# Performance work log

Measured on AMD Instinct MI355X. Metric: run time of the kernel, lower is better.

Reference implementation:

```python
import jax, jax.numpy as jnp
from jax import lax
import numpy as np

# ---- constants (from Coords2Elec init kwargs) ----
BOX = 128          # box_size
RES = 1.0          # resolution (Angstrom / voxel)
EPS_IN = 6.5
EPS_OUT = 79.0
ION = 1.0          # ion_size
WAT = 1.4          # wat_size (water probe radius)
ASIGMA = 2.0
KAPPA02 = 0.8486   # debye_length kwarg, passed to solver as kappa0^2
QCONV = 7046.52    # charge_conv
D = 2              # gaussian sharpness divisor
W = 9              # scatter support window per axis (covers ~2.7 sigma)
N_ITER = 20        # Jacobi sweeps for the Poisson-Boltzmann solve

# staggered-grid offsets for the 4 eps channels: face-centered x/y/z + ion grid
OFFSETS = ((0.5, 0.0, 0.0), (0.0, 0.5, 0.0), (0.0, 0.0, 0.5), (0.5, 0.5, 0.5))


def _scatter_gauss(coords, sigma, mask, offset):
    """Scatter per-atom Gaussian density onto a staggered [B,BOX,BOX,BOX] grid.
    coords [B,N,3], sigma [B,N], mask [B,N], offset: 3 floats in voxel units."""
    B, N, _ = coords.shape
    off = jnp.asarray(offset, coords.dtype)
    offs = jnp.arange(W)
    # window base index so that grid node positions (idx+off)*RES bracket the atom
    base = jnp.floor(coords / RES - off).astype(jnp.int32) - W // 2     # [B,N,3]
    idx = base[..., None] + offs                                         # [B,N,3,W]
    gpos = (idx.astype(coords.dtype) + off[None, None, :, None]) * RES   # [B,N,3,W]
    d2 = (gpos - coords[..., None]) ** 2
    wax = jnp.exp(-d2 / (2.0 * sigma[:, :, None, None] ** 2))            # [B,N,3,W]
    w = (wax[:, :, 0, :, None, None] * wax[:, :, 1, None, :, None]
         * wax[:, :, 2, None, None, :]) * mask[:, :, None, None, None]   # [B,N,W,W,W]
    b_idx = jnp.broadcast_to(jnp.arange(B)[:, None, None, None, None], w.shape)
    ix = jnp.broadcast_to(idx[:, :, 0, :, None, None], w.shape)
    iy = jnp.broadcast_to(idx[:, :, 1, None, :, None], w.shape)
    iz = jnp.broadcast_to(idx[:, :, 2, None, None, :], w.shape)
    grid = jnp.zeros((B, BOX, BOX, BOX), coords.dtype)
    return grid.at[b_idx, ix, iy, iz].add(w, mode='drop')


def _scatter_q(coords, charge, mask):
    """Trilinear scatter of per-atom charges onto node grid [B,BOX,BOX,BOX]."""
    B, N, _ = coords.shape
    u = coords / RES
    i0 = jnp.floor(u).astype(jnp.int32)                 # [B,N,3]
    f = u - i0
    wpair = jnp.stack([1.0 - f, f], -1)                 # [B,N,3,2]
    ipair = jnp.stack([i0, i0 + 1], -1)                 # [B,N,3,2]
    w = (wpair[:, :, 0, :, None, None] * wpair[:, :, 1, None, :, None]
         * wpair[:, :, 2, None, None, :]) * (charge * mask)[:, :, None, None, None]
    b_idx = jnp.broadcast_to(jnp.arange(B)[:, None, None, None, None], w.shape)
    ix = jnp.broadcast_to(ipair[:, :, 0, :, None, None], w.shape)
    iy = jnp.broadcast_to(ipair[:, :, 1, None, :, None], w.shape)
    iz = jnp.broadcast_to(ipair[:, :, 2, None, None, :], w.shape)
    grid = jnp.zeros((B, BOX, BOX, BOX), coords.dtype)
    return grid.at[b_idx, ix, iy, iz].add(w, mode='drop')


def _face_nb(a, axis):
    """Face eps of the (i-1) cell along axis; boundary padded with EPS_OUT."""
    lead = jnp.full_like(lax.slice_in_dim(a, 0, 1, axis=axis), EPS_OUT)
    return jnp.concatenate([lead, lax.slice_in_dim(a, 0, a.shape[axis] - 1, axis=axis)], axis=axis)


def _phi_nb(phi, axis, d):
    """Neighbor potential phi[i+d] along spatial axis, zero (Dirichlet) outside."""
    z = jnp.zeros_like(lax.slice_in_dim(phi, 0, 1, axis=axis))
    if d > 0:
        return jnp.concatenate([lax.slice_in_dim(phi, 1, phi.shape[axis], axis=axis), z], axis=axis)
    return jnp.concatenate([z, lax.slice_in_dim(phi, 0, phi.shape[axis] - 1, axis=axis)], axis=axis)


def _qeps2phi(Q, Eps):
    """Fixed-iteration Jacobi solve of the linearized Poisson-Boltzmann stencil."""
    ex, ey, ez, ek = Eps[:, 0], Eps[:, 1], Eps[:, 2], Eps[:, 3]
    exm, eym, ezm = _face_nb(ex, 1), _face_nb(ey, 2), _face_nb(ez, 3)
    lam = jnp.clip((ek - EPS_IN) / (EPS_OUT - EPS_IN), 0.0, 1.0)  # ion accessibility
    denom = ex + exm + ey + eym + ez + ezm + KAPPA02 * RES * RES * lam
    src = 4.0 * jnp.pi * Q * RES

    def body(i, phi):
        num = (ex * _phi_nb(phi, 1, +1) + exm * _phi_nb(phi, 1, -1)
               + ey * _phi_nb(phi, 2, +1) + eym * _phi_nb(phi, 2, -1)
               + ez * _phi_nb(phi, 3, +1) + ezm * _phi_nb(phi, 3, -1) + src)
        return num / denom

    return lax.fori_loop(0, N_ITER, body, jnp.zeros_like(Q))


def setup_inputs() -> dict:
    key = jax.random.key(0)
    k1, k2, k3, k4 = jax.random.split(key, 4)
    B, N = 4, 4096
    coords = jax.random.uniform(k1, (B, N, 3), jnp.float32) * ((BOX - 1) * RES)
    charges = jax.random.normal(k2, (B, N), jnp.float32) * 0.5     # partial charges
    radii = 1.0 + jax.random.uniform(k3, (B, N), jnp.float32)      # 1..2 Angstrom
    assigned_params = jnp.stack([charges, radii], -1)              # [B,N,2]
    num_atoms = jax.random.randint(k4, (B,), N // 2, N + 1, jnp.int32)
    return {"coords": coords, "assigned_params": assigned_params, "num_atoms": num_atoms}


def reference(coords, assigned_params, num_atoms):
    B, N, _ = coords.shape
    mask = (jnp.arange(N)[None, :] < num_atoms[:, None]).astype(coords.dtype)
    charge = assigned_params[..., 0]
    radii = assigned_params[..., 1]
    sig_eps = (radii + WAT) / D   # solvent-excluded Gaussian width
    sig_ion = (radii + ION) / D   # ion-excluded Gaussian width
    rho = jnp.stack([
        _scatter_gauss(coords, sig_eps if c < 3 else sig_ion, mask, OFFSETS[c])
        for c in range(4)], axis=1)                     # [B,4,BOX,BOX,BOX]
    rho = jnp.clip(rho, 0.0, 1.0)
    eps = rho * (EPS_IN - EPS_OUT) + EPS_OUT
    q = _scatter_q(coords, charge, mask) * QCONV        # [B,BOX,BOX,BOX]
    phi = _qeps2phi(q, eps)
    return q, eps, phi
```

## Files before the change

kernel.cpp:

```cpp
#include <hip/hip_runtime.h>
#include <hip/hip_fp16.h>
#include <math.h>

static constexpr int   B_    = 4;
static constexpr int   N_    = 4096;
static constexpr int   BOX_  = 128;
static constexpr long long VOX_ = 1LL * BOX_ * BOX_ * BOX_;
static constexpr float EPS_IN_C  = 6.5f;
static constexpr float EPS_OUT_C = 79.0f;
static constexpr float QCONV_C   = 7046.52f;
static constexpr float KAPPA02_C = 0.8486f;
static constexpr float FOURPI_C  = 12.566370614359172f;

__global__ void scatter_q_kernel(const float* __restrict__ coords,
                                 const float* __restrict__ params,
                                 const int*   __restrict__ num_atoms,
                                 float* __restrict__ q)
{
    int a = blockIdx.x * blockDim.x + threadIdx.x;
    if (a >= B_ * N_) return;
    int b = a >> 12;
    int n = a & (N_ - 1);
    if (n >= num_atoms[b]) return;

    float cx = coords[3 * a + 0];
    float cy = coords[3 * a + 1];
    float cz = coords[3 * a + 2];
    float chg = params[2 * a + 0] * QCONV_C;

    int ix0 = (int)floorf(cx), iy0 = (int)floorf(cy), iz0 = (int)floorf(cz);
    float fx = cx - (float)ix0, fy = cy - (float)iy0, fz = cz - (float)iz0;
    float wx[2] = {1.0f - fx, fx};
    float wy[2] = {1.0f - fy, fy};
    float wz[2] = {1.0f - fz, fz};

    float* qb = q + (long long)b * VOX_;
#pragma unroll
    for (int dx = 0; dx < 2; ++dx) {
        int ix = ix0 + dx;
        if ((unsigned)ix >= 128u) continue;
#pragma unroll
        for (int dy = 0; dy < 2; ++dy) {
            int iy = iy0 + dy;
            if ((unsigned)iy >= 128u) continue;
#pragma unroll
            for (int dz = 0; dz < 2; ++dz) {
                int iz = iz0 + dz;
                if ((unsigned)iz >= 128u) continue;
                atomicAdd(&qb[((long long)ix * 128 + iy) * 128 + iz],
                          chg * wx[dx] * wy[dy] * wz[dz]);
            }
        }
    }
}

#define CAND_CAP 512
#define CHUNK 32

__global__ __launch_bounds__(512)
void eps_gather_v3(const float* __restrict__ coords,
                   const float* __restrict__ params,
                   const int*   __restrict__ num_atoms,
                   float* __restrict__ eps)
{
    int bid = blockIdx.x;
    int b   = bid >> 8;
    int txi = (bid >> 4) & 15;
    int tyi = bid & 15;
    int tx = txi << 3, ty = tyi << 3;

    __shared__ float sx[CAND_CAP], sy[CAND_CAP], sz[CAND_CAP], sr[CAND_CAP];
    __shared__ float wts[CHUNK][9][8];
    __shared__ int  fidx[CAND_CAP];
    __shared__ int  s_cnt, s_fcnt;
    if (threadIdx.x == 0) s_cnt = 0;
    __syncthreads();

    int na = num_atoms[b];
    const float* cb = coords + (size_t)b * N_ * 3;
    const float* pb = params + (size_t)b * N_ * 2;

    float lox = (float)tx - 4.0f, hix = (float)tx + 12.5f;
    float loy = (float)ty - 4.0f, hiy = (float)ty + 12.5f;
    bool wx_ = (tx == 120), wy_ = (ty == 120);
    for (int n = threadIdx.x; n < na; n += 512) {
        float cx = cb[3 * n], cy = cb[3 * n + 1], cz = cb[3 * n + 2];
        bool okx = (cx >= lox && cx < hix) || (wx_ && cx < 4.5f);
        bool oky = (cy >= loy && cy < hiy) || (wy_ && cy < 4.5f);
        if (okx && oky) {
            int slot = atomicAdd(&s_cnt, 1);
            if (slot < CAND_CAP) {
                sx[slot] = cx; sy[slot] = cy; sz[slot] = cz;
                sr[slot] = pb[2 * n + 1];
            }
        }
    }
    __syncthreads();
    int cnt = min(s_cnt, CAND_CAP);

    int lz = threadIdx.x & 7;
    int ly = (threadIdx.x >> 3) & 7;
    int lx = threadIdx.x >> 6;

    float* eb = eps + (size_t)b * 4 * VOX_;

    for (int tzi = 0; tzi < 16; ++tzi) {
        int tz = tzi << 3;

        __syncthreads();
        if (threadIdx.x == 0) s_fcnt = 0;
        __syncthreads();
        {
            float loz = (float)tz - 4.0f, hiz = (float)tz + 12.5f;
            bool wz_ = (tz == 120);
            for (int i = threadIdx.x; i < cnt; i += 512) {
                float cz = sz[i];
                if ((cz >= loz && cz < hiz) || (wz_ && cz < 4.5f)) {
                    int s = atomicAdd(&s_fcnt, 1);
                    fidx[s] = i;
                }
            }
        }
        __syncthreads();
        int fcnt = s_fcnt;

        float r0 = 0.0f, r1 = 0.0f, r2 = 0.0f, r3 = 0.0f;

        for (int k0 = 0; k0 < fcnt; k0 += CHUNK) {
            int nC = min(CHUNK, fcnt - k0);
            __syncthreads();
            for (int w = threadIdx.x; w < nC * 72; w += 512) {
                int ka  = w / 72;
                int rem = w - ka * 72;
                int vi  = rem >> 3;
                int pos = rem & 7;
                int axis = vi / 3, var = vi - axis * 3;
                int k = fidx[k0 + ka];
                float c     = (axis == 0) ? sx[k] : (axis == 1) ? sy[k] : sz[k];
                int   torig = (axis == 0) ? tx    : (axis == 1) ? ty    : tz;
                float r = sr[k];
                float sig = (var == 2) ? (r + 1.0f) * 0.5f : (r + 1.4f) * 0.5f;
                float off = (var == 0) ? 0.0f : 0.5f;
                float inv2s2 = 1.0f / (2.0f * sig * sig);
                int i = torig + pos;
                int base = (int)floorf(c - off) - 4;
                float wv = 0.0f;
                if ((unsigned)(i - base) <= 8u) {
                    float d = (float)i + off - c;
                    wv = expf(-d * d * inv2s2);
                } else if ((unsigned)(i - 128 - base) <= 8u) {
                    float d = (float)(i - 128) + off - c;
                    wv = expf(-d * d * inv2s2);
                }
                wts[ka][vi][pos] = wv;
            }
            __syncthreads();
            for (int ka = 0; ka < nC; ++ka) {
                float xE0 = wts[ka][0][lx], xE5 = wts[ka][1][lx], xI5 = wts[ka][2][lx];
                float yE0 = wts[ka][3][ly], yE5 = wts[ka][4][ly], yI5 = wts[ka][5][ly];
                float zE0 = wts[ka][6][lz], zE5 = wts[ka][7][lz], zI5 = wts[ka][8][lz];
                r0 += xE5 * yE0 * zE0;
                r1 += xE0 * yE5 * zE0;
                r2 += xE0 * yE0 * zE5;
                r3 += xI5 * yI5 * zI5;
            }
        }

        int ix = tx + lx, iy = ty + ly, iz = tz + lz;
        size_t sp = ((size_t)ix * 128 + iy) * 128 + iz;
        eb[sp]                    = EPS_OUT_C + (EPS_IN_C - EPS_OUT_C) * fminf(fmaxf(r0, 0.0f), 1.0f);
        eb[sp + (size_t)VOX_]     = EPS_OUT_C + (EPS_IN_C - EPS_OUT_C) * fminf(fmaxf(r1, 0.0f), 1.0f);
        eb[sp + (size_t)VOX_ * 2] = EPS_OUT_C + (EPS_IN_C - EPS_OUT_C) * fminf(fmaxf(r2, 0.0f), 1.0f);
        eb[sp + (size_t)VOX_ * 3] = EPS_OUT_C + (EPS_IN_C - EPS_OUT_C) * fminf(fmaxf(r3, 0.0f), 1.0f);
    }
}

__global__ void coef_pack4(const float* __restrict__ eps,
                           const float* __restrict__ q,
                           uint4* __restrict__ coef,
                           float* __restrict__ phi1)
{
    int tid = blockIdx.x * blockDim.x + threadIdx.x;
    size_t g4 = (size_t)tid * 4;
    int b  = (int)(g4 >> 21);
    size_t sp = g4 & (size_t)(VOX_ - 1);
    int x  = (int)(sp >> 14);
    int y  = (int)((sp >> 7) & 127);
    int z4 = (int)(sp & 127);

    const float* E = eps + (size_t)b * 4 * (size_t)VOX_;
    float4 ex4 = *reinterpret_cast<const float4*>(E + sp);
    float4 ey4 = *reinterpret_cast<const float4*>(E + sp + (size_t)VOX_);
    float4 ez4 = *reinterpret_cast<const float4*>(E + sp + (size_t)VOX_ * 2);
    float4 ek4 = *reinterpret_cast<const float4*>(E + sp + (size_t)VOX_ * 3);
    float4 eo  = make_float4(EPS_OUT_C, EPS_OUT_C, EPS_OUT_C, EPS_OUT_C);
    float4 exm4 = (x > 0) ? *reinterpret_cast<const float4*>(E + sp - 16384) : eo;
    float4 eym4 = (y > 0) ? *reinterpret_cast<const float4*>(E + sp + (size_t)VOX_ - 128) : eo;
    float ezm0  = (z4 > 0) ? E[sp + (size_t)VOX_ * 2 - 1] : EPS_OUT_C;
    float4 q4  = *reinterpret_cast<const float4*>(q + g4);

    float exA[4]  = {ex4.x, ex4.y, ex4.z, ex4.w};
    float eyA[4]  = {ey4.x, ey4.y, ey4.z, ey4.w};
    float ezA[4]  = {ez4.x, ez4.y, ez4.z, ez4.w};
    float ekA[4]  = {ek4.x, ek4.y, ek4.z, ek4.w};
    float exmA[4] = {exm4.x, exm4.y, exm4.z, exm4.w};
    float eymA[4] = {eym4.x, eym4.y, eym4.z, eym4.w};
    float ezmA[4] = {ezm0, ez4.x, ez4.y, ez4.z};
    float qA[4]   = {q4.x, q4.y, q4.z, q4.w};

    float ph[4];
#pragma unroll
    for (int j = 0; j < 4; ++j) {
        float lam = (ekA[j] - EPS_IN_C) / (EPS_OUT_C - EPS_IN_C);
        lam = fminf(fmaxf(lam, 0.0f), 1.0f);
        float denom = exA[j] + exmA[j] + eyA[j] + eymA[j] + ezA[j] + ezmA[j]
                    + KAPPA02_C * lam;
        float rcp = 1.0f / denom;

        __half2 h01 = __floats2half2_rn(exA[j] * rcp, exmA[j] * rcp);
        __half2 h23 = __floats2half2_rn(eyA[j] * rcp, eymA[j] * rcp);
        __half2 h45 = __floats2half2_rn(ezA[j] * rcp, ezmA[j] * rcp);
        __half2 h67 = __floats2half2_rn(FOURPI_C * qA[j] * rcp, 0.0f);
        uint4 u;
        u.x = *(unsigned int*)&h01;
        u.y = *(unsigned int*)&h23;
        u.z = *(unsigned int*)&h45;
        u.w = *(unsigned int*)&h67;
        coef[g4 + j] = u;
        ph[j] = __half22float2(h67).x;
    }
    *reinterpret_cast<float4*>(phi1 + g4) = make_float4(ph[0], ph[1], ph[2], ph[3]);
}

#define TY 16
#define TZ 32
#define RY (TY + 2)
#define RZ (TZ + 2)
#define PYD (TY + 4)
#define PZD (TZ + 4)
#define SEG 16

__global__ __launch_bounds__(512)
void jacobi_f2p(const uint4* __restrict__ coef,
                const float* __restrict__ pin,
                float* __restrict__ pout)
{
    int bid = blockIdx.x;
    int xs = bid & 7;
    int zt = (bid >> 3) & 3;
    int yt = (bid >> 5) & 7;
    int b  = bid >> 8;
    int x_lo = xs * SEG, x_hi = x_lo + SEG - 1;
    int y0 = yt * TY, z0 = zt * TZ;

    __shared__ float P[3][PYD * PZD];
    __shared__ float S[3][RY * RZ];

    int tid = threadIdx.x;
    int oy = tid >> 5, oz = tid & 31;

    const uint4* cb = coef + (size_t)b * VOX_;
    const float* pb = pin  + (size_t)b * VOX_;
    float*       ob = pout + (size_t)b * VOX_;

    int e1_i  = (oy + 1) * RZ + (oz + 1);
    int g1y = y0 + oy, g1z = z0 + oz;
    int e1_off = g1y * 128 + g1z;
    int e1_p0 = (oy + 2) * PZD + (oz + 2);
    bool has2 = (tid < 100);
    int e2_ry = 0, e2_rz = 0;
    if (tid < 34)       { e2_ry = 0;      e2_rz = tid; }
    else if (tid < 68)  { e2_ry = RY - 1; e2_rz = tid - 34; }
    else if (tid < 100) { int t2 = tid - 68; e2_ry = 1 + (t2 >> 1); e2_rz = (t2 & 1) * (RZ - 1); }
    int e2_i = e2_ry * RZ + e2_rz;
    int g2y = y0 - 1 + e2_ry, g2z = z0 - 1 + e2_rz;
    bool e2_ok = ((unsigned)g2y < 128u) && ((unsigned)g2z < 128u);
    int e2_off = min(max(g2y, 0), 127) * 128 + min(max(g2z, 0), 127);
    int e2_p0 = (e2_ry + 1) * PZD + (e2_rz + 1);
    int p1_py = tid / PZD, p1_pz = tid - p1_py * PZD;
    int p1y = y0 - 2 + p1_py, p1z = z0 - 2 + p1_pz;
    bool p1_ok = ((unsigned)p1y < 128u) && ((unsigned)p1z < 128u);
    int p1_off = min(max(p1y, 0), 127) * 128 + min(max(p1z, 0), 127);
    int p2i = tid + 512;
    bool hasP2 = (p2i < PYD * PZD);
    int p2_py = p2i / PZD, p2_pz = p2i - p2_py * PZD;
    int p2y = y0 - 2 + p2_py, p2z = z0 - 2 + p2_pz;
    bool p2_ok = hasP2 && ((unsigned)p2y < 128u) && ((unsigned)p2z < 128u);
    int p2_off = min(max(p2y, 0), 127) * 128 + min(max(p2z, 0), 127);

    const float* ps0 = pb + (size_t)min(max(x_lo - 2, 0), 127) * 16384;
    float pfA = ps0[p1_off];
    float pfB = hasP2 ? ps0[p2_off] : 0.0f;
    uint4 cf1 = make_uint4(0u, 0u, 0u, 0u);
    uint4 cf2 = make_uint4(0u, 0u, 0u, 0u);
    uint4 hold = make_uint4(0u, 0u, 0u, 0u);
    uint4 cnew = make_uint4(0u, 0u, 0u, 0u);

    for (int x = x_lo - 2; x <= x_hi + 2; ++x) {
        int s0 = (x + 3) % 3;
        int s1 = (x + 2) % 3;
        int s2 = (x + 1) % 3;
        bool xin = (x >= 0 && x < 128);

        P[s0][tid] = (xin && p1_ok) ? pfA : 0.0f;
        if (hasP2) P[s0][p2i] = (xin && p2_ok) ? pfB : 0.0f;
        asm volatile("s_waitcnt lgkmcnt(0)" ::: "memory");
        __builtin_amdgcn_s_barrier();

        if (x < x_hi + 2) {
            const float* ps = pb + (size_t)min(max(x + 1, 0), 127) * 16384;
            pfA = ps[p1_off];
            if (hasP2) pfB = ps[p2_off];
        }

        if (x >= x_lo) {
            int k = x - 1;
            bool kin = ((unsigned)k < 128u);
            {
                float v = 0.0f;
                if (kin) {
                    const __half2* h = reinterpret_cast<const __half2*>(&cf1);
                    float2 a01 = __half22float2(h[0]);
                    float2 a23 = __half22float2(h[1]);
                    float2 a45 = __half22float2(h[2]);
                    float2 a67 = __half22float2(h[3]);
                    v = a01.x * P[s0][e1_p0]
                      + a01.y * P[s2][e1_p0]
                      + a23.x * P[s1][e1_p0 + PZD]
                      + a23.y * P[s1][e1_p0 - PZD]
                      + a45.x * P[s1][e1_p0 + 1]
                      + a45.y * P[s1][e1_p0 - 1]
                      + a67.x;
                }
                S[s1][e1_i] = v;
                cnew = cf1;
            }
            if (has2) {
                float v = 0.0f;
                if (kin && e2_ok) {
                    const __half2* h = reinterpret_cast<const __half2*>(&cf2);
                    float2 a01 = __half22float2(h[0]);
                    float2 a23 = __half22float2(h[1]);
                    float2 a45 = __half22float2(h[2]);
                    float2 a67 = __half22float2(h[3]);
                    v = a01.x * P[s0][e2_p0]
                      + a01.y * P[s2][e2_p0]
                      + a23.x * P[s1][e2_p0 + PZD]
                      + a23.y * P[s1][e2_p0 - PZD]
                      + a45.x * P[s1][e2_p0 + 1]
                      + a45.y * P[s1][e2_p0 - 1]
                      + a67.x;
                }
                S[s1][e2_i] = v;
            }
        }
        if (x >= x_lo - 1 && x <= x_hi + 1) {
            const uint4* cs = cb + (size_t)min(max(x, 0), 127) * 16384;
            cf1 = cs[e1_off];
            if (has2) cf2 = cs[e2_off];
        }
        asm volatile("s_waitcnt lgkmcnt(0)" ::: "memory");
        __builtin_amdgcn_s_barrier();

        int xo = x - 2;
        if (xo >= x_lo) {
            const __half2* h = reinterpret_cast<const __half2*>(&hold);
            float2 a01 = __half22float2(h[0]);
            float2 a23 = __half22float2(h[1]);
            float2 a45 = __half22float2(h[2]);
            float2 a67 = __half22float2(h[3]);
            int j0 = e1_i;
            float out = a01.x * S[s1][j0]
                      + a01.y * S[s0][j0]
                      + a23.x * S[s2][j0 + RZ]
                      + a23.y * S[s2][j0 - RZ]
                      + a45.x * S[s2][j0 + 1]
                      + a45.y * S[s2][j0 - 1]
                      + a67.x;
            ob[(size_t)xo * 16384 + e1_off] = out;
        }
        hold = cnew;
    }
}

__global__ void jacobi_v3(const uint4* __restrict__ coef,
                          const float* __restrict__ pin,
                          float* __restrict__ pout)
{
    int tid = blockIdx.x * blockDim.x + threadIdx.x;
    size_t g4 = (size_t)tid * 4;
    int z4 = (int)(g4 & 127);
    int y  = (int)((g4 >> 7) & 127);
    int x  = (int)((g4 >> 14) & 127);

    float4 pcv = *reinterpret_cast<const float4*>(pin + g4);
    float4 z4v = make_float4(0.f, 0.f, 0.f, 0.f);
    float4 pxpv = (x < 127) ? *reinterpret_cast<const float4*>(pin + g4 + 16384) : z4v;
    float4 pxmv = (x > 0)   ? *reinterpret_cast<const float4*>(pin + g4 - 16384) : z4v;
    float4 pypv = (y < 127) ? *reinterpret_cast<const float4*>(pin + g4 + 128)   : z4v;
    float4 pymv = (y > 0)   ? *reinterpret_cast<const float4*>(pin + g4 - 128)   : z4v;
    float zpE = (z4 < 124) ? pin[g4 + 4] : 0.0f;
    float zmE = (z4 > 0)   ? pin[g4 - 1] : 0.0f;

    float pxp[4] = {pxpv.x, pxpv.y, pxpv.z, pxpv.w};
    float pxm[4] = {pxmv.x, pxmv.y, pxmv.z, pxmv.w};
    float pyp[4] = {pypv.x, pypv.y, pypv.z, pypv.w};
    float pym[4] = {pymv.x, pymv.y, pymv.z, pymv.w};
    float pzp[4] = {pcv.y, pcv.z, pcv.w, zpE};
    float pzm[4] = {zmE, pcv.x, pcv.y, pcv.z};

    float out[4];
#pragma unroll
    for (int j = 0; j < 4; ++j) {
        uint4 cu = coef[g4 + j];
        const __half2* h = reinterpret_cast<const __half2*>(&cu);
        float2 a01 = __half22float2(h[0]);
        float2 a23 = __half22float2(h[1]);
        float2 a45 = __half22float2(h[2]);
        float2 a67 = __half22float2(h[3]);
        out[j] = a01.x * pxp[j] + a01.y * pxm[j]
               + a23.x * pyp[j] + a23.y * pym[j]
               + a45.x * pzp[j] + a45.y * pzm[j]
               + a67.x;
    }
    *reinterpret_cast<float4*>(pout + g4) = make_float4(out[0], out[1], out[2], out[3]);
}

__global__ void jacobi_v2(const float* __restrict__ eps,
                          const float* __restrict__ q,
                          const float* __restrict__ pin,
                          float* __restrict__ pout)
{
    int bxy = blockIdx.x;
    int b = bxy >> 14;
    int x = (bxy >> 7) & 127;
    int y = bxy & 127;
    int z = threadIdx.x;

    size_t sp = ((size_t)x * 128 + y) * 128 + z;
    size_t g  = (size_t)b * (size_t)VOX_ + sp;
    const float* E = eps + (size_t)b * 4 * (size_t)VOX_;

    float ex = E[sp];
    float ey = E[sp + (size_t)VOX_];
    float ez = E[sp + (size_t)VOX_ * 2];
    float ek = E[sp + (size_t)VOX_ * 3];
    float exm = (x > 0) ? E[sp - 16384]                 : EPS_OUT_C;
    float eym = (y > 0) ? E[sp + (size_t)VOX_ - 128]    : EPS_OUT_C;
    float ezm = (z > 0) ? E[sp + (size_t)VOX_ * 2 - 1]  : EPS_OUT_C;

    float lam = (ek - EPS_IN_C) / (EPS_OUT_C - EPS_IN_C);
    lam = fminf(fmaxf(lam, 0.0f), 1.0f);
    float denom = ex + exm + ey + eym + ez + ezm + KAPPA02_C * lam;

    float pxp = (x < 127) ? pin[g + 16384] : 0.0f;
    float pxm = (x > 0)   ? pin[g - 16384] : 0.0f;
    float pyp = (y < 127) ? pin[g + 128]   : 0.0f;
    float pym = (y > 0)   ? pin[g - 128]   : 0.0f;
    float pzp = (z < 127) ? pin[g + 1]     : 0.0f;
    float pzm = (z > 0)   ? pin[g - 1]     : 0.0f;

    float num = ex * pxp + exm * pxm + ey * pyp + eym * pym
              + ez * pzp + ezm * pzm + FOURPI_C * q[g];
    pout[g] = num / denom;
}

extern "C" void kernel_launch(void* const* d_in, const int* in_sizes, int n_in,
                              void* d_out, int out_size, void* d_ws, size_t ws_size,
                              hipStream_t stream)
{
    const float* coords    = (const float*)d_in[0];
    const float* params    = (const float*)d_in[1];
    const int*   num_atoms = (const int*)d_in[2];

    float* q   = (float*)d_out;
    float* eps = q + (size_t)B_ * VOX_;
    float* phi = eps + (size_t)B_ * 4 * VOX_;

    hipMemsetAsync(q, 0, (size_t)B_ * VOX_ * sizeof(float), stream);

    scatter_q_kernel<<<(B_ * N_ + 255) / 256, 256, 0, stream>>>(coords, params, num_atoms, q);
    eps_gather_v3<<<B_ * 16 * 16, 512, 0, stream>>>(coords, params, num_atoms, eps);

    size_t coefBytes = (size_t)B_ * VOX_ * sizeof(uint4);
    size_t need = coefBytes + (size_t)B_ * VOX_ * sizeof(float);

    if (ws_size >= need) {
        uint4* coefA = (uint4*)d_ws;
        float* tmp   = (float*)((char*)d_ws + coefBytes);
        coef_pack4<<<(int)(B_ * VOX_ / 4 / 256), 256, 0, stream>>>(eps, q, coefA, phi);
        const float* cur = phi;
        for (int it = 1; it <= 9; ++it) {
            float* dst = (it & 1) ? tmp : phi;
            jacobi_f2p<<<B_ * 8 * 4 * 8, 512, 0, stream>>>(coefA, cur, dst);
            cur = dst;
        }
        jacobi_v3<<<(int)(B_ * VOX_ / 4 / 256), 256, 0, stream>>>(coefA, cur, phi);
    } else {
        hipMemsetAsync(phi, 0, (size_t)B_ * VOX_ * sizeof(float), stream);
        float* tmp = (float*)d_ws;
        int jb = B_ * 128 * 128;
        const float* cur = phi;
        for (int it = 1; it <= 20; ++it) {
            float* dst = (it & 1) ? tmp : phi;
            jacobi_v2<<<jb, 128, 0, stream>>>(eps, q, cur, dst);
            cur = dst;
        }
    }
}
```

Baseline: 724.4 us.

## Fuse three Jacobi sweeps per kernel with deeper temporal blocking

Replaces the two-sweep temporally blocked Jacobi kernel with a three-sweep version that keeps two intermediate planes in shared memory. Boundary-ring coefficients are staged through shared memory so they can be reused across stages. The iteration count drops from nine launches to six, keeping the total number of sweeps the same. The goal is to cut global memory traffic and launch count, at the price of a wider halo, more redundant boundary compute, an extra barrier per plane and more shared memory per block, which may reduce occupancy.

```diff
diff --git a/kernel.cpp b/kernel.cpp
--- a/kernel.cpp
+++ b/kernel.cpp
@@ -232,29 +232,34 @@
     *reinterpret_cast<float4*>(phi1 + g4) = make_float4(ph[0], ph[1], ph[2], ph[3]);
 }
 
-#define TY 16
-#define TZ 32
-#define RY (TY + 2)
-#define RZ (TZ + 2)
-#define PYD (TY + 4)
-#define PZD (TZ + 4)
-#define SEG 16
+#define TY3 16
+#define TZ3 32
+#define R1Y 20
+#define R1Z 36
+#define R2Y 18
+#define R2Z 34
+#define PY3 22
+#define PZ3 38
+#define SEG3 16
+#define NBND 208
 
 __global__ __launch_bounds__(512)
-void jacobi_f2p(const uint4* __restrict__ coef,
-                const float* __restrict__ pin,
-                float* __restrict__ pout)
+void jacobi_f3(const uint4* __restrict__ coef,
+               const float* __restrict__ pin,
+               float* __restrict__ pout)
 {
     int bid = blockIdx.x;
     int xs = bid & 7;
     int zt = (bid >> 3) & 3;
     int yt = (bid >> 5) & 7;
     int b  = bid >> 8;
-    int x_lo = xs * SEG, x_hi = x_lo + SEG - 1;
-    int y0 = yt * TY, z0 = zt * TZ;
-
-    __shared__ float P[3][PYD * PZD];
-    __shared__ float S[3][RY * RZ];
+    int x_lo = xs * SEG3, x_hi = x_lo + SEG3 - 1;
+    int y0 = yt * TY3, z0 = zt * TZ3;
+
+    __shared__ float P [3][PY3 * PZ3];
+    __shared__ float S1[3][R1Y * R1Z];
+    __shared__ float S2[3][R2Y * R2Z];
+    __shared__ uint4 CFB[3][NBND];
 
     int tid = threadIdx.x;
     int oy = tid >> 5, oz = tid & 31;
@@ -263,123 +268,184 @@
     const float* pb = pin  + (size_t)b * VOX_;
     float*       ob = pout + (size_t)b * VOX_;
 
-    int e1_i  = (oy + 1) * RZ + (oz + 1);
-    int g1y = y0 + oy, g1z = z0 + oz;
-    int e1_off = g1y * 128 + g1z;
-    int e1_p0 = (oy + 2) * PZD + (oz + 2);
-    bool has2 = (tid < 100);
-    int e2_ry = 0, e2_rz = 0;
-    if (tid < 34)       { e2_ry = 0;      e2_rz = tid; }
-    else if (tid < 68)  { e2_ry = RY - 1; e2_rz = tid - 34; }
-    else if (tid < 100) { int t2 = tid - 68; e2_ry = 1 + (t2 >> 1); e2_rz = (t2 & 1) * (RZ - 1); }
-    int e2_i = e2_ry * RZ + e2_rz;
-    int g2y = y0 - 1 + e2_ry, g2z = z0 - 1 + e2_rz;
-    bool e2_ok = ((unsigned)g2y < 128u) && ((unsigned)g2z < 128u);
-    int e2_off = min(max(g2y, 0), 127) * 128 + min(max(g2z, 0), 127);
-    int e2_p0 = (e2_ry + 1) * PZD + (e2_rz + 1);
-    int p1_py = tid / PZD, p1_pz = tid - p1_py * PZD;
-    int p1y = y0 - 2 + p1_py, p1z = z0 - 2 + p1_pz;
+    int off_c = (y0 + oy) * 128 + (z0 + oz);
+    int i2_c  = (oy + 1) * R2Z + (oz + 1);
+    int i1_c  = (oy + 2) * R1Z + (oz + 2);
+    int ip_c  = (oy + 3) * PZ3 + (oz + 3);
+
+    bool hasB = (tid < NBND);
+    bool isB1 = (tid < 100);
+    int r2y = 0, r2z = 0, r1y = 0, r1z = 0;
+    if (tid < 34)        { r2y = 0;  r2z = tid; }
+    else if (tid < 68)   { r2y = 17; r2z = tid - 34; }
+    else if (tid < 100)  { int t = tid - 68; r2y = 1 + (t >> 1); r2z = (t & 1) ? 33 : 0; }
+    if (isB1) { r1y = r2y + 1; r1z = r2z + 1; }
+    else if (hasB) {
+        int t2 = tid - 100;
+        if (t2 < 36)      { r1y = 0;  r1z = t2; }
+        else if (t2 < 72) { r1y = 19; r1z = t2 - 36; }
+        else              { int t = t2 - 72; r1y = 1 + (t >> 1); r1z = (t & 1) ? 35 : 0; }
+    }
+    int bnd_i1 = r1y * R1Z + r1z;
+    int bnd_ip = (r1y + 1) * PZ3 + (r1z + 1);
+    int bgy = y0 - 2 + r1y, bgz = z0 - 2 + r1z;
+    bool bnd_ok = ((unsigned)bgy < 128u) && ((unsigned)bgz < 128u);
+    int bnd_off = min(max(bgy, 0), 127) * 128 + min(max(bgz, 0), 127);
+    int i2_b1 = r2y * R2Z + r2z;
+
+    int p1_py = tid / PZ3, p1_pz = tid - p1_py * PZ3;
+    int p1y = y0 - 3 + p1_py, p1z = z0 - 3 + p1_pz;
     bool p1_ok = ((unsigned)p1y < 128u) && ((unsigned)p1z < 128u);
     int p1_off = min(max(p1y, 0), 127) * 128 + min(max(p1z, 0), 127);
     int p2i = tid + 512;
-    bool hasP2 = (p2i < PYD * PZD);
-    int p2_py = p2i / PZD, p2_pz = p2i - p2_py * PZD;
-    int p2y = y0 - 2 + p2_py, p2z = z0 - 2 + p2_pz;
+    bool hasP2 = (p2i < PY3 * PZ3);
+    int p2_py = p2i / PZ3, p2_pz = p2i - p2_py * PZ3;
+    int p2y = y0 - 3 + p2_py, p2z = z0 - 3 + p2_pz;
     bool p2_ok = hasP2 && ((unsigned)p2y < 128u) && ((unsigned)p2z < 128u);
     int p2_off = min(max(p2y, 0), 127) * 128 + min(max(p2z, 0), 127);
 
-    const float* ps0 = pb + (size_t)min(max(x_lo - 2, 0), 127) * 16384;
+    const float* ps0 = pb + (size_t)min(max(x_lo - 3, 0), 127) * 16384;
     float pfA = ps0[p1_off];
     float pfB = hasP2 ? ps0[p2_off] : 0.0f;
-    uint4 cf1 = make_uint4(0u, 0u, 0u, 0u);
-    uint4 cf2 = make_uint4(0u, 0u, 0u, 0u);
-    uint4 hold = make_uint4(0u, 0u, 0u, 0u);
-    uint4 cnew = make_uint4(0u, 0u, 0u, 0u);
-
-    for (int x = x_lo - 2; x <= x_hi + 2; ++x) {
-        int s0 = (x + 3) % 3;
-        int s1 = (x + 2) % 3;
-        int s2 = (x + 1) % 3;
+    uint4 z4 = make_uint4(0u, 0u, 0u, 0u);
+    uint4 cfn = z4, cf_b1 = z4, cf_b2 = z4, cf_c = z4, cfbn = z4;
+
+    for (int x = x_lo - 3; x <= x_hi + 3; ++x) {
+        int m0 = (x + 6) % 3;
+        int m1 = (x + 5) % 3;
+        int m2 = (x + 4) % 3;
         bool xin = (x >= 0 && x < 128);
 
-        P[s0][tid] = (xin && p1_ok) ? pfA : 0.0f;
-        if (hasP2) P[s0][p2i] = (xin && p2_ok) ? pfB : 0.0f;
+        P[m0][tid] = (xin && p1_ok) ? pfA : 0.0f;
+        if (hasP2) P[m0][p2i] = (xin && p2_ok) ? pfB : 0.0f;
+        if (hasB) CFB[m1][tid] = cfbn;
         asm volatile("s_waitcnt lgkmcnt(0)" ::: "memory");
         __builtin_amdgcn_s_barrier();
 
-        if (x < x_hi + 2) {
+        if (x < x_hi + 3) {
             const float* ps = pb + (size_t)min(max(x + 1, 0), 127) * 16384;
             pfA = ps[p1_off];
             if (hasP2) pfB = ps[p2_off];
         }
 
-        if (x >= x_lo) {
-            int k = x - 1;
-            bool kin = ((unsigned)k < 128u);
-            {
-                float v = 0.0f;
-                if (kin) {
-                    const __half2* h = reinterpret_cast<const __half2*>(&cf1);
-                    float2 a01 = __half22float2(h[0]);
-                    float2 a23 = __half22float2(h[1]);
-                    float2 a45 = __half22float2(h[2]);
-                    float2 a67 = __half22float2(h[3]);
-                    v = a01.x * P[s0][e1_p0]
-                      + a01.y * P[s2][e1_p0]
-                      + a23.x * P[s1][e1_p0 + PZD]
-                      + a23.y * P[s1][e1_p0 - PZD]
-                      + a45.x * P[s1][e1_p0 + 1]
-                      + a45.y * P[s1][e1_p0 - 1]
-                      + a67.x;
+        {
+            int k1 = x - 1;
+            if (k1 >= x_lo - 2 && k1 <= x_hi + 2) {
+                bool kin = ((unsigned)k1 < 128u);
+                {
+                    float v = 0.0f;
+                    if (kin) {
+                        const __half2* h = reinterpret_cast<const __half2*>(&cf_b1);
+                        float2 a01 = __half22float2(h[0]);
+                        float2 a23 = __half22float2(h[1]);
+                        float2 a45 = __half22float2(h[2]);
+                        float2 a67 = __half22float2(h[3]);
+                        v = a01.x * P[m0][ip_c]
+                          + a01.y * P[m2][ip_c]
+                          + a23.x * P[m1][ip_c + PZ3]
+                          + a23.y * P[m1][ip_c - PZ3]
+                          + a45.x * P[m1][ip_c + 1]
+                          + a45.y * P[m1][ip_c - 1]
+                          + a67.x;
+                    }
+                    S1[m1][i1_c] = v;
                 }
-                S[s1][e1_i] = v;
-                cnew = cf1;
-            }
-            if (has2) {
-                float v = 0.0f;
-                if (kin && e2_ok) {
-                    const __half2* h = reinterpret_cast<const __half2*>(&cf2);
-                    float2 a01 = __half22float2(h[0]);
-                    float2 a23 = __half22float2(h[1]);
-                    float2 a45 = __half22float2(h[2]);
-                    float2 a67 = __half22float2(h[3]);
-                    v = a01.x * P[s0][e2_p0]
-                      + a01.y * P[s2][e2_p0]
-                      + a23.x * P[s1][e2_p0 + PZD]
-                      + a23.y * P[s1][e2_p0 - PZD]
-                      + a45.x * P[s1][e2_p0 + 1]
-                      + a45.y * P[s1][e2_p0 - 1]
-                      + a67.x;
+                if (hasB) {
+                    float v = 0.0f;
+                    if (kin && bnd_ok) {
+                        uint4 cu = CFB[m1][tid];
+                        const __half2* h = reinterpret_cast<const __half2*>(&cu);
+                        float2 a01 = __half22float2(h[0]);
+                        float2 a23 = __half22float2(h[1]);
+                        float2 a45 = __half22float2(h[2]);
+                        float2 a67 = __half22float2(h[3]);
+                        v = a01.x * P[m0][bnd_ip]
+                          + a01.y * P[m2][bnd_ip]
+                          + a23.x * P[m1][bnd_ip + PZ3]
+                          + a23.y * P[m1][bnd_ip - PZ3]
+                          + a45.x * P[m1][bnd_ip + 1]
+                          + a45.y * P[m1][bnd_ip - 1]
+                          + a67.x;
+                    }
+                    S1[m1][bnd_i1] = v;
                 }
-                S[s1][e2_i] = v;
-            }
-        }
-        if (x >= x_lo - 1 && x <= x_hi + 1) {
+            }
+        }
+        if (x >= x_lo - 2 && x <= x_hi + 2) {
             const uint4* cs = cb + (size_t)min(max(x, 0), 127) * 16384;
-            cf1 = cs[e1_off];
-            if (has2) cf2 = cs[e2_off];
+            cfn = cs[off_c];
+            if (hasB) cfbn = cs[bnd_off];
         }
         asm volatile("s_waitcnt lgkmcnt(0)" ::: "memory");
         __builtin_amdgcn_s_barrier();
 
-        int xo = x - 2;
-        if (xo >= x_lo) {
-            const __half2* h = reinterpret_cast<const __half2*>(&hold);
-            float2 a01 = __half22float2(h[0]);
-            float2 a23 = __half22float2(h[1]);
-            float2 a45 = __half22float2(h[2]);
-            float2 a67 = __half22float2(h[3]);
-            int j0 = e1_i;
-            float out = a01.x * S[s1][j0]
-                      + a01.y * S[s0][j0]
-                      + a23.x * S[s2][j0 + RZ]
-                      + a23.y * S[s2][j0 - RZ]
-                      + a45.x * S[s2][j0 + 1]
-                      + a45.y * S[s2][j0 - 1]
-                      + a67.x;
-            ob[(size_t)xo * 16384 + e1_off] = out;
-        }
-        hold = cnew;
+        {
+            int k2 = x - 2;
+            if (k2 >= x_lo - 1 && k2 <= x_hi + 1) {
+                bool kin = ((unsigned)k2 < 128u);
+                {
+                    float v = 0.0f;
+                    if (kin) {
+                        const __half2* h = reinterpret_cast<const __half2*>(&cf_b2);
+                        float2 a01 = __half22float2(h[0]);
+                        float2 a23 = __half22float2(h[1]);
+                        float2 a45 = __half22float2(h[2]);
+                        float2 a67 = __half22float2(h[3]);
+                        v = a01.x * S1[m1][i1_c]
+                          + a01.y * S1[m0][i1_c]
+                          + a23.x * S1[m2][i1_c + R1Z]
+                          + a23.y * S1[m2][i1_c - R1Z]
+                          + a45.x * S1[m2][i1_c + 1]
+                          + a45.y * S1[m2][i1_c - 1]
+                          + a67.x;
+                    }
+                    S2[m2][i2_c] = v;
+                }
+                if (isB1) {
+                    float v = 0.0f;
+                    if (kin && bnd_ok) {
+                        uint4 cu = CFB[m2][tid];
+                        const __half2* h = reinterpret_cast<const __half2*>(&cu);
+                        float2 a01 = __half22float2(h[0]);
+                        float2 a23 = __half22float2(h[1]);
+                        float2 a45 = __half22float2(h[2]);
+                        float2 a67 = __half22float2(h[3]);
+                        v = a01.x * S1[m1][bnd_i1]
+                          + a01.y * S1[m0][bnd_i1]
+                          + a23.x * S1[m2][bnd_i1 + R1Z]
+                          + a23.y * S1[m2][bnd_i1 - R1Z]
+                          + a45.x * S1[m2][bnd_i1 + 1]
+                          + a45.y * S1[m2][bnd_i1 - 1]
+                          + a67.x;
+                    }
+                    S2[m2][i2_b1] = v;
+                }
+            }
+        }
+        asm volatile("s_waitcnt lgkmcnt(0)" ::: "memory");
+        __builtin_amdgcn_s_barrier();
+
+        {
+            int xo = x - 3;
+            if (xo >= x_lo) {
+                const __half2* h = reinterpret_cast<const __half2*>(&cf_c);
+                float2 a01 = __half22float2(h[0]);
+                float2 a23 = __half22float2(h[1]);
+                float2 a45 = __half22float2(h[2]);
+                float2 a67 = __half22float2(h[3]);
+                float out = a01.x * S2[m2][i2_c]
+                          + a01.y * S2[m1][i2_c]
+                          + a23.x * S2[m0][i2_c + R2Z]
+                          + a23.y * S2[m0][i2_c - R2Z]
+                          + a45.x * S2[m0][i2_c + 1]
+                          + a45.y * S2[m0][i2_c - 1]
+                          + a67.x;
+                ob[(size_t)xo * 16384 + off_c] = out;
+            }
+        }
+        cf_c  = cf_b2;
+        cf_b2 = cf_b1;
+        cf_b1 = cfn;
     }
 }
 
@@ -488,11 +554,11 @@
     if (ws_size >= need) {
         uint4* coefA = (uint4*)d_ws;
         float* tmp   = (float*)((char*)d_ws + coefBytes);
-        coef_pack4<<<(int)(B_ * VOX_ / 4 / 256), 256, 0, stream>>>(eps, q, coefA, phi);
-        const float* cur = phi;
-        for (int it = 1; it <= 9; ++it) {
-            float* dst = (it & 1) ? tmp : phi;
-            jacobi_f2p<<<B_ * 8 * 4 * 8, 512, 0, stream>>>(coefA, cur, dst);
+        coef_pack4<<<(int)(B_ * VOX_ / 4 / 256), 256, 0, stream>>>(eps, q, coefA, tmp);
+        const float* cur = tmp;
+        for (int it = 1; it <= 6; ++it) {
+            float* dst = (it & 1) ? phi : tmp;
+            jacobi_f3<<<B_ * 8 * 8 * 4, 512, 0, stream>>>(coefA, cur, dst);
             cur = dst;
         }
         jacobi_v3<<<(int)(B_ * VOX_ / 4 / 256), 256, 0, stream>>>(coefA, cur, phi);
```

After: 763.3 us. 5.4% more time.
